# Optimization experiments

Hardware: AMD Instinct MI355X
Metric: run time of the kernel (lower is better)

Reference implementation:

```python
import jax, jax.numpy as jnp
import numpy as np

NEG_SLOPE = 0.2  # PyG GATv2Conv default leaky_relu slope


def _gatv2(x, src, dst, eattr, Wl, bl, Wr, br, We, att, bias, N):
    """GATv2Conv (concat heads, eval mode -> no dropout).
    x: [N, Fin], src/dst: [E], eattr: [E, Fe], att: [H, C]."""
    H, C = att.shape
    xl = (x @ Wl.T + bl).reshape(N, H, C)   # lin_l -> source features
    xr = (x @ Wr.T + br).reshape(N, H, C)   # lin_r -> target features
    ea = (eattr @ We.T).reshape(-1, H, C)   # lin_edge (no bias)
    m = xl[src] + xr[dst] + ea              # [E, H, C]
    m = jnp.where(m >= 0, m, NEG_SLOPE * m)
    logits = jnp.einsum('ehc,hc->eh', m, att)  # [E, H]
    # segment softmax over incoming edges of each target node
    lmax = jax.ops.segment_max(logits, dst, num_segments=N)  # self-loops -> nonempty
    ex = jnp.exp(logits - lmax[dst])
    denom = jax.ops.segment_sum(ex, dst, num_segments=N)
    alpha = ex / denom[dst]                 # [E, H]
    out = jax.ops.segment_sum(alpha[:, :, None] * xl[src], dst, num_segments=N)
    return out.reshape(N, H * C) + bias


def setup_inputs() -> dict:
    key = jax.random.key(0)
    ks = jax.random.split(key, 24)
    B, num_nodes, Fn, Fe, deg = 16, 5000, 64, 16, 32
    N = B * num_nodes
    E = N * deg
    s = 0.05
    inp = {
        'x': jax.random.normal(ks[0], (N, Fn), jnp.float32),
        'edge_index': jax.random.randint(ks[1], (2, E), 0, N, jnp.int64),
        'edge_attr': jax.random.normal(ks[2], (E, Fe), jnp.float32),
        'num_nodes': num_nodes,
        'W1l': jax.random.normal(ks[3], (9, Fn), jnp.float32) * s,
        'b1l': jnp.zeros((9,), jnp.float32),
        'W1r': jax.random.normal(ks[4], (9, Fn), jnp.float32) * s,
        'b1r': jnp.zeros((9,), jnp.float32),
        'We1': jax.random.normal(ks[5], (9, Fe), jnp.float32) * s,
        'att1': jax.random.normal(ks[6], (3, 3), jnp.float32) * s,
        'bias1': jnp.zeros((9,), jnp.float32),
        'W2l': jax.random.normal(ks[7], (20, 9), jnp.float32) * s,
        'b2l': jnp.zeros((20,), jnp.float32),
        'W2r': jax.random.normal(ks[8], (20, 9), jnp.float32) * s,
        'b2r': jnp.zeros((20,), jnp.float32),
        'We2': jax.random.normal(ks[9], (20, Fe), jnp.float32) * s,
        'att2': jax.random.normal(ks[10], (4, 5), jnp.float32) * s,
        'bias2': jnp.zeros((20,), jnp.float32),
        'fcW1': jax.random.normal(ks[11], (100, 20 * num_nodes), jnp.float32) * 0.01,
        'fcb1': jnp.zeros((100,), jnp.float32),
        'fcW2': jax.random.normal(ks[12], (10, 100), jnp.float32) * s,
        'fcb2': jnp.zeros((10,), jnp.float32),
        'fcW3': jax.random.normal(ks[13], (1, 10), jnp.float32) * s,
        'fcb3': jnp.zeros((1,), jnp.float32),
    }
    return inp


def reference(x, edge_index, edge_attr, num_nodes,
              W1l, b1l, W1r, b1r, We1, att1, bias1,
              W2l, b2l, W2r, b2r, We2, att2, bias2,
              fcW1, fcb1, fcW2, fcb2, fcW3, fcb3):
    N = x.shape[0]
    src0, dst0 = edge_index[0], edge_index[1]
    # add_self_loops=True, fill_value='mean': loop attr = mean of incoming edge attrs
    cnt = jax.ops.segment_sum(jnp.ones((src0.shape[0],), x.dtype), dst0, num_segments=N)
    loop_attr = jax.ops.segment_sum(edge_attr, dst0, num_segments=N) / jnp.maximum(cnt, 1.0)[:, None]
    nodes = jnp.arange(N)
    src = jnp.concatenate([src0, nodes])
    dst = jnp.concatenate([dst0, nodes])
    ea = jnp.concatenate([edge_attr, loop_attr], axis=0)

    h = _gatv2(x, src, dst, ea, W1l, b1l, W1r, b1r, We1, att1, bias1, N)
    h = jax.nn.relu(h)
    h = _gatv2(h, src, dst, ea, W2l, b2l, W2r, b2r, We2, att2, bias2, N)
    h = jax.nn.relu(h)

    B = N // num_nodes
    h = h.reshape(B, num_nodes * 20)
    h = jax.nn.relu(h @ fcW1.T + fcb1)
    h = jax.nn.relu(h @ fcW2.T + fcb2)
    return h @ fcW3.T + fcb3
```

## Files before the change

kernel.cpp:

```cpp
#include <hip/hip_runtime.h>
#include <math.h>

#define TPB   256
#define NPB   256
#define MAXNB 512
#define BCAP  10240
#define ITEMS 32
#define CPAD  16

static inline int gridFor(size_t n) { return (int)((n + TPB - 1) / TPB); }


__global__ void __launch_bounds__(TPB) k_lin1(
    const float* __restrict__ x,
    const float* __restrict__ Wl, const float* __restrict__ bl,
    const float* __restrict__ Wr, const float* __restrict__ br,
    float* __restrict__ xl, float* __restrict__ xr, int N)
{
  int idx = blockIdx.x * TPB + threadIdx.x;
  if (idx >= N * 18) return;
  int i = idx / 18, t = idx % 18;
  bool left = t < 9;
  int j = left ? t : t - 9;
  const float* W = (left ? Wl : Wr) + j * 64;
  float s = (left ? bl : br)[j];
  const float* xi = x + (size_t)i * 64;
#pragma unroll
  for (int f = 0; f < 64; f++) s = fmaf(xi[f], W[f], s);
  (left ? xl : xr)[(size_t)i * 9 + j] = s;
}

__global__ void __launch_bounds__(TPB) k_lin2(
    const float* __restrict__ h1, const float* __restrict__ bias1,
    const float* __restrict__ Wl, const float* __restrict__ bl,
    const float* __restrict__ Wr, const float* __restrict__ br,
    float* __restrict__ xl, float* __restrict__ xr, int N)
{
  int idx = blockIdx.x * TPB + threadIdx.x;
  if (idx >= N * 40) return;
  int i = idx / 40, t = idx % 40;
  float hr[9];
#pragma unroll
  for (int k = 0; k < 9; k++) hr[k] = fmaxf(h1[(size_t)i * 9 + k] + bias1[k], 0.0f);
  bool left = t < 20;
  int j = left ? t : t - 20;
  const float* W = (left ? Wl : Wr) + j * 9;
  float s = (left ? bl : br)[j];
#pragma unroll
  for (int k = 0; k < 9; k++) s = fmaf(hr[k], W[k], s);
  (left ? xl : xr)[(size_t)i * 20 + j] = s;
}


__global__ void __launch_bounds__(TPB) k_bin(
    const int* __restrict__ ei, int* __restrict__ bucketCntP,
    int2* __restrict__ staging, int E, int NB)
{
  __shared__ int hist[MAXNB];
  __shared__ int base[MAXNB];
  int tid = threadIdx.x;
  size_t tile0 = (size_t)blockIdx.x * (TPB * ITEMS);
  for (int i = tid; i < NB; i += TPB) hist[i] = 0;
  __syncthreads();
  for (int it = 0; it < ITEMS; ++it) {
    size_t e = tile0 + (size_t)it * TPB + tid;
    if (e < (size_t)E) {
      int dst = ei[(size_t)E + e];
      atomicAdd(&hist[dst >> 8], 1);
    }
  }
  __syncthreads();
  for (int i = tid; i < NB; i += TPB) {
    int c = hist[i];
    base[i] = c ? atomicAdd(&bucketCntP[(size_t)i * CPAD], c) : 0;
    hist[i] = 0;
  }
  __syncthreads();
  for (int it = 0; it < ITEMS; ++it) {
    size_t e = tile0 + (size_t)it * TPB + tid;
    if (e < (size_t)E) {
      int src = ei[e];
      int dst = ei[(size_t)E + e];
      int b = dst >> 8;
      int r = atomicAdd(&hist[b], 1);
      staging[(size_t)b * BCAP + base[b] + r] =
          make_int2((int)e | ((dst & 255) << 22), src);
    }
  }
}


__global__ void __launch_bounds__(MAXNB) k_scanb(
    const int* __restrict__ bucketCntP, int* __restrict__ bucketBase, int NB)
{
  __shared__ int s[MAXNB];
  int tid = threadIdx.x;
  int v = (tid < NB) ? bucketCntP[(size_t)tid * CPAD] : 0;
  s[tid] = v;
  __syncthreads();
  for (int off = 1; off < MAXNB; off <<= 1) {
    int u = (tid >= off) ? s[tid - off] : 0;
    __syncthreads();
    s[tid] += u;
    __syncthreads();
  }
  if (tid < NB) bucketBase[tid] = s[tid] - v;
}


__global__ void __launch_bounds__(TPB) k_csr(
    const int2* __restrict__ staging, const int* __restrict__ bucketCntP,
    const int* __restrict__ bucketBase,
    int* __restrict__ rowptr, int* __restrict__ degO,
    int* __restrict__ src_csr, int* __restrict__ eid_csr, int N)
{
  int b = blockIdx.x, tid = threadIdx.x;
  int n0 = b << 8;
  int recCnt = bucketCntP[(size_t)b * CPAD];
  int ebase = bucketBase[b];
  const int2* rec = staging + (size_t)b * BCAP;
  __shared__ int deg_s[NPB];
  __shared__ int pfx[NPB];
  __shared__ int cur[NPB];
  deg_s[tid] = 0;
  __syncthreads();
  for (int r = tid; r < recCnt; r += TPB)
    atomicAdd(&deg_s[(rec[r].x >> 22) & 255], 1);
  __syncthreads();
  pfx[tid] = deg_s[tid];
  __syncthreads();
  for (int off = 1; off < NPB; off <<= 1) {
    int u = (tid >= off) ? pfx[tid - off] : 0;
    __syncthreads();
    pfx[tid] += u;
    __syncthreads();
  }
  int excl = pfx[tid] - deg_s[tid];
  int n = n0 + tid;
  if (n < N) { rowptr[n] = ebase + excl; degO[n] = deg_s[tid]; }
  cur[tid] = ebase + excl;
  __syncthreads();
  for (int r = tid; r < recCnt; r += TPB) {
    int2 rc = rec[r];
    int dl = (rc.x >> 22) & 255;
    int eid = rc.x & 0x3FFFFF;
    int pos = atomicAdd(&cur[dl], 1);
    src_csr[pos] = rc.y;
    eid_csr[pos] = eid;
  }
}


__global__ void __launch_bounds__(TPB) k_reorder(
    const int* __restrict__ eid_csr, const float* __restrict__ eattr,
    float4* __restrict__ eac, int E)
{
  int slot = blockIdx.x * TPB + threadIdx.x;
  if (slot >= E) return;
  const float4* s = (const float4*)(eattr + (size_t)eid_csr[slot] * 16);
  float4* d = eac + (size_t)slot * 4;
  d[0] = s[0]; d[1] = s[1]; d[2] = s[2]; d[3] = s[3];
}


template <int H, int C, bool SEQ>
__global__ void __launch_bounds__(TPB) k_attn(
    const int* __restrict__ rowptr, const int* __restrict__ deg,
    const int* __restrict__ src_csr, const int* __restrict__ eid_csr,
    const float* __restrict__ ea_src,
    const float* __restrict__ xl, const float* __restrict__ xr,
    const float* __restrict__ We, const float* __restrict__ att,
    const float* __restrict__ bias,
    float* __restrict__ out, int N)
{
  constexpr int HC = H * C;
  int idx = blockIdx.x * TPB + threadIdx.x;
  if (idx >= N * H) return;
  int n = idx / H, h = idx % H;

  float w[C][16];
#pragma unroll
  for (int c = 0; c < C; c++)
#pragma unroll
    for (int f = 0; f < 16; f++) w[c][f] = We[(h * C + c) * 16 + f];
  float attv[C], xrv[C];
#pragma unroll
  for (int c = 0; c < C; c++) {
    attv[c] = att[h * C + c];
    xrv[c] = xr[(size_t)n * HC + h * C + c];
  }

  int r0 = rowptr[n];
  int dg = deg[n];

  float mx = -INFINITY, den = 0.0f;
  float acc[C], ea_sum[C];
#pragma unroll
  for (int c = 0; c < C; c++) { acc[c] = 0.0f; ea_sum[c] = 0.0f; }

  for (int p = 0; p < dg; p++) {
    int pos = r0 + p;
    size_t abase = SEQ ? (size_t)pos * 16 : (size_t)eid_csr[pos] * 16;
    float a[16];
    const float4* a4 = (const float4*)(ea_src + abase);
#pragma unroll
    for (int k = 0; k < 4; k++) {
      float4 v = a4[k];
      a[4 * k + 0] = v.x; a[4 * k + 1] = v.y; a[4 * k + 2] = v.z; a[4 * k + 3] = v.w;
    }
    int srcn = src_csr[pos];
    const float* xs = xl + (size_t)srcn * HC + h * C;
    float xv[C];
#pragma unroll
    for (int c = 0; c < C; c++) xv[c] = xs[c];
    float lg = 0.0f;
#pragma unroll
    for (int c = 0; c < C; c++) {
      float ea = 0.0f;
#pragma unroll
      for (int f = 0; f < 16; f++) ea = fmaf(a[f], w[c][f], ea);
      ea_sum[c] += ea;
      float m = xv[c] + xrv[c] + ea;
      m = (m >= 0.0f) ? m : 0.2f * m;
      lg = fmaf(m, attv[c], lg);
    }
    float nm = fmaxf(mx, lg);
    float s = expf(mx - nm);
    float wE = expf(lg - nm);
    den = den * s + wE;
#pragma unroll
    for (int c = 0; c < C; c++) acc[c] = fmaf(acc[c], s, wE * xv[c]);
    mx = nm;
  }

  {
    float invd = 1.0f / fmaxf((float)dg, 1.0f);
    const float* xs = xl + (size_t)n * HC + h * C;
    float xv[C];
#pragma unroll
    for (int c = 0; c < C; c++) xv[c] = xs[c];
    float lg = 0.0f;
#pragma unroll
    for (int c = 0; c < C; c++) {
      float m = xv[c] + xrv[c] + ea_sum[c] * invd;
      m = (m >= 0.0f) ? m : 0.2f * m;
      lg = fmaf(m, attv[c], lg);
    }
    float nm = fmaxf(mx, lg);
    float s = expf(mx - nm);
    float wE = expf(lg - nm);
    den = den * s + wE;
#pragma unroll
    for (int c = 0; c < C; c++) acc[c] = fmaf(acc[c], s, wE * xv[c]);
  }

  float inv = 1.0f / den;
  float* od = out + (size_t)n * HC + h * C;
#pragma unroll
  for (int c = 0; c < C; c++) {
    float v = acc[c] * inv;
    if (bias) v = fmaxf(v + bias[h * C + c], 0.0f);
    od[c] = v;
  }
}


__global__ void __launch_bounds__(TPB) k_fc1(
    const float* __restrict__ h2, const float* __restrict__ W,
    float* __restrict__ h3, int NN, int Kc)
{
  int o = blockIdx.x;
  int ks = blockIdx.y;
  int k0 = ks * Kc;
  int k1 = min(NN, k0 + Kc);
  float acc[16];
#pragma unroll
  for (int b = 0; b < 16; b++) acc[b] = 0.0f;
  const float* wo = W + (size_t)o * NN;
  for (int k = k0 + threadIdx.x; k < k1; k += TPB) {
    float w = wo[k];
#pragma unroll
    for (int b = 0; b < 16; b++) acc[b] = fmaf(h2[(size_t)b * NN + k], w, acc[b]);
  }
#pragma unroll
  for (int b = 0; b < 16; b++) {
    float v = acc[b];
#pragma unroll
    for (int off = 32; off > 0; off >>= 1) v += __shfl_down(v, off, 64);
    if ((threadIdx.x & 63) == 0) atomicAdd(&h3[b * 100 + o], v);
  }
}

__global__ void __launch_bounds__(TPB) k_fc23(
    const float* __restrict__ h3, const float* __restrict__ fcb1,
    const float* __restrict__ W2, const float* __restrict__ b2,
    const float* __restrict__ W3, const float* __restrict__ b3,
    float* __restrict__ out, int B)
{
  __shared__ float s3[32 * 100];
  __shared__ float s4[32 * 10];
  int tid = threadIdx.x;
  for (int t = tid; t < B * 100; t += TPB)
    s3[t] = fmaxf(h3[t] + fcb1[t % 100], 0.0f);
  __syncthreads();
  if (tid < B * 10) {
    int b = tid / 10, o = tid % 10;
    float s = b2[o];
#pragma unroll
    for (int k = 0; k < 100; k++) s = fmaf(s3[b * 100 + k], W2[o * 100 + k], s);
    s4[tid] = fmaxf(s, 0.0f);
  }
  __syncthreads();
  if (tid < B) {
    float s = b3[0];
#pragma unroll
    for (int k = 0; k < 10; k++) s = fmaf(s4[tid * 10 + k], W3[k], s);
    out[tid] = s;
  }
}


extern "C" void kernel_launch(void* const* d_in, const int* in_sizes, int n_in,
                              void* d_out, int out_size, void* d_ws, size_t ws_size,
                              hipStream_t stream) {
  const float* x      = (const float*)d_in[0];
  const int*   ei     = (const int*)d_in[1];
  const float* eattr  = (const float*)d_in[2];
  const float* W1l = (const float*)d_in[4];  const float* b1l = (const float*)d_in[5];
  const float* W1r = (const float*)d_in[6];  const float* b1r = (const float*)d_in[7];
  const float* We1 = (const float*)d_in[8];  const float* att1 = (const float*)d_in[9];
  const float* bias1 = (const float*)d_in[10];
  const float* W2l = (const float*)d_in[11]; const float* b2l = (const float*)d_in[12];
  const float* W2r = (const float*)d_in[13]; const float* b2r = (const float*)d_in[14];
  const float* We2 = (const float*)d_in[15]; const float* att2 = (const float*)d_in[16];
  const float* bias2 = (const float*)d_in[17];
  const float* fcW1 = (const float*)d_in[18]; const float* fcb1 = (const float*)d_in[19];
  const float* fcW2 = (const float*)d_in[20]; const float* fcb2 = (const float*)d_in[21];
  const float* fcW3 = (const float*)d_in[22]; const float* fcb3 = (const float*)d_in[23];
  float* out = (float*)d_out;

  const int N = in_sizes[0] / 64;
  const int E = in_sizes[2] / 16;
  const int num_nodes = in_sizes[18] / (100 * 20);
  const int B = N / num_nodes;
  const int NB = (N + NPB - 1) / NPB;

  char* base = (char*)d_ws;
  size_t off = 0;
  auto alloc = [&](size_t bytes) {
    size_t o = off; off += (bytes + 63) & ~(size_t)63; return o;
  };
  size_t o_bcnt   = alloc((size_t)NB * CPAD * 4);
  size_t o_h3     = alloc((size_t)B * 100 * 4);
  size_t zeroBytes = off;
  size_t o_bbase  = alloc((size_t)NB * 4);
  size_t o_stage  = alloc((size_t)NB * BCAP * 8);
  size_t o_rowptr = alloc((size_t)N * 4);
  size_t o_deg    = alloc((size_t)N * 4);
  size_t o_srcc   = alloc((size_t)E * 4);
  size_t o_eidc   = alloc((size_t)E * 4);
  size_t o_xl1    = alloc((size_t)N * 9 * 4);
  size_t o_xr1    = alloc((size_t)N * 9 * 4);
  size_t o_xl2    = alloc((size_t)N * 20 * 4);
  size_t o_xr2    = alloc((size_t)N * 20 * 4);
  size_t o_h1     = alloc((size_t)N * 9 * 4);
  size_t o_h2     = alloc((size_t)N * 20 * 4);
  size_t o_eac    = alloc((size_t)E * 16 * 4);
  bool seq = (off <= ws_size);

  int*   bcnt   = (int*)(base + o_bcnt);
  float* h3     = (float*)(base + o_h3);
  int*   bbase  = (int*)(base + o_bbase);
  int2*  stage  = (int2*)(base + o_stage);
  int*   rowptr = (int*)(base + o_rowptr);
  int*   deg    = (int*)(base + o_deg);
  int*   srcc   = (int*)(base + o_srcc);
  int*   eidc   = (int*)(base + o_eidc);
  float* xl1    = (float*)(base + o_xl1);
  float* xr1    = (float*)(base + o_xr1);
  float* xl2    = (float*)(base + o_xl2);
  float* xr2    = (float*)(base + o_xr2);
  float* h1     = (float*)(base + o_h1);
  float* h2     = (float*)(base + o_h2);
  float* eac    = (float*)(base + o_eac);

  hipMemsetAsync(d_ws, 0, zeroBytes, stream);

  k_lin1<<<gridFor((size_t)N * 18), TPB, 0, stream>>>(x, W1l, b1l, W1r, b1r, xl1, xr1, N);

  int binBlocks = (int)(((size_t)E + TPB * ITEMS - 1) / (TPB * ITEMS));
  k_bin<<<binBlocks, TPB, 0, stream>>>(ei, bcnt, stage, E, NB);
  k_scanb<<<1, MAXNB, 0, stream>>>(bcnt, bbase, NB);
  k_csr<<<NB, TPB, 0, stream>>>(stage, bcnt, bbase, rowptr, deg, srcc, eidc, N);
  if (seq)
    k_reorder<<<gridFor((size_t)E), TPB, 0, stream>>>(eidc, eattr, (float4*)eac, E);

  if (seq)
    k_attn<3, 3, true><<<gridFor((size_t)N * 3), TPB, 0, stream>>>(
        rowptr, deg, srcc, eidc, eac, xl1, xr1, We1, att1, nullptr, h1, N);
  else
    k_attn<3, 3, false><<<gridFor((size_t)N * 3), TPB, 0, stream>>>(
        rowptr, deg, srcc, eidc, eattr, xl1, xr1, We1, att1, nullptr, h1, N);

  k_lin2<<<gridFor((size_t)N * 40), TPB, 0, stream>>>(h1, bias1, W2l, b2l, W2r, b2r, xl2, xr2, N);

  if (seq)
    k_attn<4, 5, true><<<gridFor((size_t)N * 4), TPB, 0, stream>>>(
        rowptr, deg, srcc, eidc, eac, xl2, xr2, We2, att2, bias2, h2, N);
  else
    k_attn<4, 5, false><<<gridFor((size_t)N * 4), TPB, 0, stream>>>(
        rowptr, deg, srcc, eidc, eattr, xl2, xr2, We2, att2, bias2, h2, N);

  const int NN = num_nodes * 20;
  const int KS = 16;
  const int Kc = (NN + KS - 1) / KS;
  dim3 g1(100, KS);
  k_fc1<<<g1, TPB, 0, stream>>>(h2, fcW1, h3, NN, Kc);
  k_fc23<<<1, TPB, 0, stream>>>(h3, fcb1, fcW2, fcb2, fcW3, fcb3, out, B);
  (void)out_size; (void)n_in;
}
```

Baseline: 832.6 us.

## Split each node-head's edge loop across 4 lanes with shuffle-merged online softmax

Each (node, head) attention task is now handled by 4 adjacent lanes. Each lane processes a strided subset of the incoming edges with its own online softmax state. The partial max, denominator, accumulators and edge-attr sums are then merged with xor shuffles, and the self-loop term is applied after the merge. This raises thread-level parallelism and memory-level parallelism for the serial, latency-bound per-edge loop, with degree around 32. The cost is 4x redundant weight loads per lane, a shuffle reduction with extra exps, and the initial max changed from -inf to a large finite negative value to avoid NaN when a lane sees no edges.

```diff
diff --git a/kernel.cpp b/kernel.cpp
--- a/kernel.cpp
+++ b/kernel.cpp
@@ -163,7 +163,7 @@
 }
 
 
-template <int H, int C, bool SEQ>
+template <int H, int C, int L, bool SEQ>
 __global__ void __launch_bounds__(TPB) k_attn(
     const int* __restrict__ rowptr, const int* __restrict__ deg,
     const int* __restrict__ src_csr, const int* __restrict__ eid_csr,
@@ -175,8 +175,10 @@
 {
   constexpr int HC = H * C;
   int idx = blockIdx.x * TPB + threadIdx.x;
-  if (idx >= N * H) return;
-  int n = idx / H, h = idx % H;
+  if (idx >= N * H * L) return;
+  int l = idx & (L - 1);
+  int g = idx / L;
+  int n = g / H, h = g - n * H;
 
   float w[C][16];
 #pragma unroll
@@ -193,12 +195,12 @@
   int r0 = rowptr[n];
   int dg = deg[n];
 
-  float mx = -INFINITY, den = 0.0f;
+  float mx = -3.0e38f, den = 0.0f;
   float acc[C], ea_sum[C];
 #pragma unroll
   for (int c = 0; c < C; c++) { acc[c] = 0.0f; ea_sum[c] = 0.0f; }
 
-  for (int p = 0; p < dg; p++) {
+  for (int p = l; p < dg; p += L) {
     int pos = r0 + p;
     size_t abase = SEQ ? (size_t)pos * 16 : (size_t)eid_csr[pos] * 16;
     float a[16];
@@ -233,6 +235,24 @@
     mx = nm;
   }
 
+#pragma unroll
+  for (int off = 1; off < L; off <<= 1) {
+    float omx  = __shfl_xor(mx, off, 64);
+    float oden = __shfl_xor(den, off, 64);
+    float nm = fmaxf(mx, omx);
+    float s1 = expf(mx - nm);
+    float s2 = expf(omx - nm);
+    den = den * s1 + oden * s2;
+#pragma unroll
+    for (int c = 0; c < C; c++) {
+      float oa = __shfl_xor(acc[c], off, 64);
+      float oe = __shfl_xor(ea_sum[c], off, 64);
+      acc[c] = acc[c] * s1 + oa * s2;
+      ea_sum[c] += oe;
+    }
+    mx = nm;
+  }
+
   {
     float invd = 1.0f / fmaxf((float)dg, 1.0f);
     const float* xs = xl + (size_t)n * HC + h * C;
@@ -256,8 +276,7 @@
 
   float inv = 1.0f / den;
   float* od = out + (size_t)n * HC + h * C;
-#pragma unroll
-  for (int c = 0; c < C; c++) {
+  for (int c = l; c < C; c += L) {
     float v = acc[c] * inv;
     if (bias) v = fmaxf(v + bias[h * C + c], 0.0f);
     od[c] = v;
@@ -396,19 +415,19 @@
     k_reorder<<<gridFor((size_t)E), TPB, 0, stream>>>(eidc, eattr, (float4*)eac, E);
 
   if (seq)
-    k_attn<3, 3, true><<<gridFor((size_t)N * 3), TPB, 0, stream>>>(
+    k_attn<3, 3, 4, true><<<gridFor((size_t)N * 3 * 4), TPB, 0, stream>>>(
         rowptr, deg, srcc, eidc, eac, xl1, xr1, We1, att1, nullptr, h1, N);
   else
-    k_attn<3, 3, false><<<gridFor((size_t)N * 3), TPB, 0, stream>>>(
+    k_attn<3, 3, 4, false><<<gridFor((size_t)N * 3 * 4), TPB, 0, stream>>>(
         rowptr, deg, srcc, eidc, eattr, xl1, xr1, We1, att1, nullptr, h1, N);
 
   k_lin2<<<gridFor((size_t)N * 40), TPB, 0, stream>>>(h1, bias1, W2l, b2l, W2r, b2r, xl2, xr2, N);
 
   if (seq)
-    k_attn<4, 5, true><<<gridFor((size_t)N * 4), TPB, 0, stream>>>(
+    k_attn<4, 5, 4, true><<<gridFor((size_t)N * 4 * 4), TPB, 0, stream>>>(
         rowptr, deg, srcc, eidc, eac, xl2, xr2, We2, att2, bias2, h2, N);
   else
-    k_attn<4, 5, false><<<gridFor((size_t)N * 4), TPB, 0, stream>>>(
+    k_attn<4, 5, 4, false><<<gridFor((size_t)N * 4 * 4), TPB, 0, stream>>>(
         rowptr, deg, srcc, eidc, eattr, xl2, xr2, We2, att2, bias2, h2, N);
 
   const int NN = num_nodes * 20;
```

Result: faster. 799.4 us (-4.0%).
